# Kernel optimization log

Measured on AMD Instinct MI355X. Metric: run time of the kernel, lower is better.

## Reference

```python
import jax, jax.numpy as jnp
import numpy as np

NUM_WORDS = 256  # max word index + 1 (sentinel row NUM_WORDS used to drop non-first-occurrence scatters)


def setup_inputs() -> dict:
    key = jax.random.key(0)
    ks = jax.random.split(key, 8)
    B, S, H, R, D, C = 16, 512, 768, 8, 512, 27
    hidden_states = jax.random.normal(ks[0], (B, S, H), jnp.float32)
    word_ids = jnp.sort(jax.random.randint(ks[1], (B, S), 0, NUM_WORDS), axis=-1)
    relations_positions = jax.random.randint(ks[2], (B, R), 0, S)
    w_rel = jax.random.normal(ks[3], (H,), jnp.float32) / np.sqrt(H).astype(np.float32)
    b_rel = jnp.zeros((1,), jnp.float32)
    w1 = jax.random.normal(ks[4], (2 * H, D), jnp.float32) / np.sqrt(2 * H).astype(np.float32)
    b1 = jnp.zeros((D,), jnp.float32)
    w2 = jax.random.normal(ks[5], (D, C), jnp.float32) / np.sqrt(D).astype(np.float32)
    b2 = jnp.zeros((C,), jnp.float32)
    return dict(hidden_states=hidden_states, word_ids=word_ids,
                relations_positions=relations_positions,
                w_rel=w_rel, b_rel=b_rel, w1=w1, b1=b1, w2=w2, b2=b2)


def reference(hidden_states, word_ids, relations_positions, w_rel, b_rel, w1, b1, w2, b2):
    B, S, H = hidden_states.shape
    # relational logits: Linear(H, 1).squeeze(-1)  -> [B, S]
    rel_logits = jnp.einsum('bsh,h->bs', hidden_states, w_rel) + b_rel

    # first_hidden_states[i, w] = hidden_states[i, j] at the FIRST token j of word w
    # (torch loop keys on word_id != prev_word_id; word_ids are monotone per row)
    first_occ = jnp.concatenate(
        [jnp.ones((B, 1), bool), word_ids[:, 1:] != word_ids[:, :-1]], axis=1)
    tgt = jnp.where(first_occ, word_ids, NUM_WORDS)  # route non-first tokens to sentinel row
    batch_idx = jnp.arange(B)[:, None]
    first_hidden = (jnp.zeros((B, NUM_WORDS + 1, H), hidden_states.dtype)
                    .at[batch_idx, tgt].set(hidden_states))[:, :NUM_WORDS]  # [B, W, H]

    # gather relation token embeddings -> [B, R, H]
    rel_hidden = jnp.take_along_axis(
        hidden_states, relations_positions[:, :, None], axis=1)

    # concat([word_embed, rel_embed]) @ w1 == word_embed @ w1[:H] + rel_embed @ w1[H:]
    h_word = jnp.einsum('bwh,hd->bwd', first_hidden, w1[:H])   # [B, W, D]
    h_rel = jnp.einsum('brh,hd->brd', rel_hidden, w1[H:])      # [B, R, D]
    hmid = jax.nn.relu(h_word[:, None, :, :] + h_rel[:, :, None, :] + b1)  # [B, R, W, D]
    role_logits = jnp.einsum('brwd,dc->brwc', hmid, w2) + b2   # [B, R, W, C]

    return rel_logits, role_logits
```

## Files before the change

kernel.cpp:

```cpp
#include <hip/hip_runtime.h>
#include <hip/hip_bf16.h>

#define BB 16
#define SS 512
#define HH 768
#define RR 8
#define DD 512
#define CC 27
#define WW 256

typedef __attribute__((ext_vector_type(8))) short short8;
typedef __attribute__((ext_vector_type(4))) float f32x4;

union PKu { unsigned short us[8]; uint4 u4; short8 s8; };

__device__ __forceinline__ unsigned short f32_to_bf16_rne(float v) {
    unsigned int u = __float_as_uint(v);
    unsigned int r = u + 0x7fffu + ((u >> 16) & 1u);
    return (unsigned short)(r >> 16);
}
__device__ __forceinline__ float bf16_to_f32(unsigned short u) {
    return __uint_as_float(((unsigned int)u) << 16);
}

__device__ __forceinline__ void glds16(const void* g, void* l) {
    __builtin_amdgcn_global_load_lds(
        (const __attribute__((address_space(1))) unsigned int*)g,
        (__attribute__((address_space(3))) unsigned int*)l, 16, 0, 0);
}


__global__ __launch_bounds__(256) void k_front(
    const float* __restrict__ hidden, const int* __restrict__ word_ids,
    const int* __restrict__ relpos, const float4* __restrict__ wrel4,
    const float* __restrict__ b_rel, const float* __restrict__ w1,
    const float* __restrict__ w2, float* __restrict__ out0,
    unsigned short* __restrict__ first_hidden,
    unsigned short* __restrict__ rel_hidden,
    unsigned short* __restrict__ w1t, unsigned short* __restrict__ w2t) {
    int bid = blockIdx.x, t = threadIdx.x;
    if (bid < 2048) {
        int lane = t & 63;
        int row = bid * 4 + (t >> 6);
        const float4* hid4 = (const float4*)hidden + (size_t)row * (HH / 4);
        float4 v[3];
        float acc = 0.f;
#pragma unroll
        for (int j = 0; j < 3; ++j) {
            v[j] = hid4[j * 64 + lane];
            float4 w = wrel4[j * 64 + lane];
            acc += v[j].x * w.x + v[j].y * w.y + v[j].z * w.z + v[j].w * w.w;
        }
#pragma unroll
        for (int off = 32; off > 0; off >>= 1) acc += __shfl_xor(acc, off, 64);
        if (lane == 0) out0[row] = acc + b_rel[0];
        int wid = word_ids[row];
        int s = row & (SS - 1);
        int prev = (s == 0) ? -1 : word_ids[row - 1];
        if (wid != prev) {
            int b = row >> 9;
            unsigned short* dst = first_hidden + (size_t)(b * WW + wid) * HH;
#pragma unroll
            for (int j = 0; j < 3; ++j) {
                union { unsigned short us[4]; uint2 u2; } pk;
                pk.us[0] = f32_to_bf16_rne(v[j].x);
                pk.us[1] = f32_to_bf16_rne(v[j].y);
                pk.us[2] = f32_to_bf16_rne(v[j].z);
                pk.us[3] = f32_to_bf16_rne(v[j].w);
                *(uint2*)(dst + j * 256 + lane * 4) = pk.u2;
            }
        }
        return;
    }
    int x = bid - 2048;
    if (x < 192) {
        __shared__ unsigned short tile[64][72];
        int kt = x >> 3, nt = x & 7;
        int i = t >> 2, j4 = (t & 3) * 16;
        const float* src = w1 + (size_t)(kt * 64 + i) * DD + nt * 64 + j4;
#pragma unroll
        for (int v = 0; v < 4; ++v) {
            float4 f = *(const float4*)(src + v * 4);
            tile[i][j4 + v * 4 + 0] = f32_to_bf16_rne(f.x);
            tile[i][j4 + v * 4 + 1] = f32_to_bf16_rne(f.y);
            tile[i][j4 + v * 4 + 2] = f32_to_bf16_rne(f.z);
            tile[i][j4 + v * 4 + 3] = f32_to_bf16_rne(f.w);
        }
        __syncthreads();
        int jj = t >> 2, cb = (t & 3) * 16;
        union { unsigned short us[16]; uint4 u4[2]; } ov;
#pragma unroll
        for (int v = 0; v < 16; ++v) ov.us[v] = tile[cb + v][jj];
        unsigned short* dst = w1t + (size_t)(nt * 64 + jj) * (2 * HH) + kt * 64 + cb;
        *(uint4*)(dst) = ov.u4[0];
        *(uint4*)(dst + 8) = ov.u4[1];
    } else if (x == 192) {
        for (int idx = t; idx < 32 * DD; idx += 256) {
            int n = idx >> 9, k = idx & (DD - 1);
            float v = (n < CC) ? w2[(size_t)k * CC + n] : 0.f;
            w2t[n * DD + k] = f32_to_bf16_rne(v);
        }
    } else {
        __shared__ int pres[WW];
        int b = x - 193;
        pres[t] = 0;
        __syncthreads();
        for (int s = t; s < SS; s += 256) pres[word_ids[b * SS + s]] = 1;
        __syncthreads();
        if (!pres[t]) {
            uint4 z = {0u, 0u, 0u, 0u};
            unsigned short* dst = first_hidden + (size_t)(b * WW + t) * HH;
#pragma unroll 4
            for (int c = 0; c < 96; ++c) *(uint4*)(dst + c * 8) = z;
        }
        for (int idx = t; idx < 1024; idx += 256) {
            int rr = idx >> 7, c = idx & 127;
            if (c < 96) {
                int pos = relpos[b * RR + rr];
                const float* srow = hidden + (size_t)(b * SS + pos) * HH + c * 8;
                PKu pk;
#pragma unroll
                for (int e = 0; e < 8; ++e) pk.us[e] = f32_to_bf16_rne(srow[e]);
                *(uint4*)(rel_hidden + (size_t)(b * RR + rr) * HH + c * 8) = pk.u4;
            }
        }
    }
}

__global__ __launch_bounds__(256) void k_gemm(
    const unsigned short* __restrict__ first_hidden,
    const unsigned short* __restrict__ rel_hidden,
    const unsigned short* __restrict__ w1t, const float* __restrict__ b1,
    unsigned short* __restrict__ h_word, unsigned short* __restrict__ h_rel) {
    __shared__ __align__(16) unsigned char a_s[32768];
    __shared__ __align__(16) unsigned char b_s[16384];
    int bid = blockIdx.x;
    int nt, mt;
    if (bid < 256) {
        int xcd = bid & 7, k = bid >> 3;
        mt = xcd + 8 * (k & 3);
        nt = k >> 2;
    } else {
        mt = 32;
        nt = bid - 256;
    }
    bool isw = (mt < 32);
    const unsigned short* A = isw ? first_hidden : rel_hidden;
    unsigned short* C = isw ? h_word : h_rel;
    int kbase = isw ? 0 : HH;
    int m0 = isw ? mt * 128 : 0;
    int t = threadIdx.x;
    int wv = t >> 6, lane = t & 63;
    int wr = wv >> 1, wc = wv & 1;
    int q = lane >> 4, r = lane & 15;

    const unsigned char* aP[4];
    const unsigned char* bP[2];
    unsigned lofa[4], lofb[2];
#pragma unroll
    for (int j = 0; j < 4; ++j) {
        int ci = j * 256 + t;
        int row = ci >> 3, ch = ci & 7;
        int sc = ch ^ (row & 7);
        aP[j] = (const unsigned char*)A + (size_t)(m0 + row) * (HH * 2) + sc * 16;
        lofa[j] = ci * 16;
    }
#pragma unroll
    for (int j = 0; j < 2; ++j) {
        int ci = j * 256 + t;
        int row = ci >> 3, ch = ci & 7;
        int sc = ch ^ (row & 7);
        bP[j] = (const unsigned char*)w1t + (size_t)(nt * 64 + row) * (2 * HH * 2)
                + (size_t)kbase * 2 + sc * 16;
        lofb[j] = ci * 16;
    }
    int arow[4], brow[2];
#pragma unroll
    for (int mi = 0; mi < 4; ++mi) arow[mi] = wr * 64 + mi * 16 + r;
#pragma unroll
    for (int ni = 0; ni < 2; ++ni) brow[ni] = wc * 32 + ni * 16 + r;

    f32x4 acc[4][2];
#pragma unroll
    for (int mi = 0; mi < 4; ++mi)
#pragma unroll
        for (int ni = 0; ni < 2; ++ni) acc[mi][ni] = (f32x4){0.f, 0.f, 0.f, 0.f};

#pragma unroll
    for (int j = 0; j < 4; ++j) glds16(aP[j], a_s + lofa[j]);
#pragma unroll
    for (int j = 0; j < 2; ++j) glds16(bP[j], b_s + lofb[j]);
    __syncthreads();

    for (int kt = 0; kt < 12; ++kt) {
        if (kt < 11) {
            unsigned na = ((kt + 1) & 1) * 16384;
            unsigned nb = ((kt + 1) & 1) * 8192;
#pragma unroll
            for (int j = 0; j < 4; ++j) glds16(aP[j] + (kt + 1) * 128, a_s + na + lofa[j]);
#pragma unroll
            for (int j = 0; j < 2; ++j) glds16(bP[j] + (kt + 1) * 128, b_s + nb + lofb[j]);
        }
        unsigned ba = (kt & 1) * 16384;
        unsigned bb = (kt & 1) * 8192;
#pragma unroll
        for (int ks = 0; ks < 2; ++ks) {
            int c = ks * 4 + q;
            short8 bfr[2];
#pragma unroll
            for (int ni = 0; ni < 2; ++ni)
                bfr[ni] = *(const short8*)(b_s + bb + brow[ni] * 128 +
                            ((c ^ (brow[ni] & 7)) << 4));
#pragma unroll
            for (int mi = 0; mi < 4; ++mi) {
                short8 af = *(const short8*)(a_s + ba + arow[mi] * 128 +
                            ((c ^ (arow[mi] & 7)) << 4));
                acc[mi][0] = __builtin_amdgcn_mfma_f32_16x16x32_bf16(
                    af, bfr[0], acc[mi][0], 0, 0, 0);
                acc[mi][1] = __builtin_amdgcn_mfma_f32_16x16x32_bf16(
                    af, bfr[1], acc[mi][1], 0, 0, 0);
            }
        }
        __syncthreads();
    }
    float bias[2];
#pragma unroll
    for (int ni = 0; ni < 2; ++ni) {
        int n = nt * 64 + wc * 32 + ni * 16 + r;
        bias[ni] = isw ? b1[n] : 0.f;
    }
#pragma unroll
    for (int mi = 0; mi < 4; ++mi) {
        int m = m0 + wr * 64 + mi * 16 + q * 4;
#pragma unroll
        for (int ni = 0; ni < 2; ++ni) {
            int n = nt * 64 + wc * 32 + ni * 16 + r;
#pragma unroll
            for (int reg = 0; reg < 4; ++reg)
                C[(size_t)(m + reg) * DD + n] =
                    f32_to_bf16_rne(acc[mi][ni][reg] + bias[ni]);
        }
    }
}

__global__ __launch_bounds__(512) void k_role(
    const unsigned short* __restrict__ h_word, const unsigned short* __restrict__ h_rel,
    const unsigned short* __restrict__ w2t, const float* __restrict__ b2,
    float* __restrict__ out_role) {
    int wt = blockIdx.x;
    int b  = blockIdx.y;
    int t  = threadIdx.x;
    __shared__ __align__(16) unsigned char hw_s[16384];
    __shared__ float hr_s[RR][DD];
    __shared__ __align__(16) unsigned char w2_s[32768];
    int wv = t >> 6, lane = t & 63;
    {
#pragma unroll
        for (int i = 0; i < 2; ++i) {
            int row = wv * 2 + i;
            const unsigned short* src = h_word +
                (size_t)(b * WW + wt * 16 + row) * DD + ((lane ^ (row & 7)) * 8);
            glds16(src, hw_s + row * 1024 + lane * 16);
        }
    }
    {
#pragma unroll
        for (int i = 0; i < 4; ++i) {
            int row = wv * 4 + i;
            const unsigned short* src = w2t + row * DD + ((lane ^ (row & 7)) * 8);
            glds16(src, w2_s + row * 1024 + lane * 16);
        }
    }
    {
        int rr = t >> 6, c = t & 63;
        PKu hv;
        hv.u4 = *(const uint4*)(h_rel + (size_t)(b * RR + rr) * DD + c * 8);
        float4 o0, o1;
        o0.x = bf16_to_f32(hv.us[0]); o0.y = bf16_to_f32(hv.us[1]);
        o0.z = bf16_to_f32(hv.us[2]); o0.w = bf16_to_f32(hv.us[3]);
        o1.x = bf16_to_f32(hv.us[4]); o1.y = bf16_to_f32(hv.us[5]);
        o1.z = bf16_to_f32(hv.us[6]); o1.w = bf16_to_f32(hv.us[7]);
        *(float4*)&hr_s[rr][c * 8]     = o0;
        *(float4*)&hr_s[rr][c * 8 + 4] = o1;
    }
    __syncthreads();
    int q = lane >> 4, wl = lane & 15;
    int rr = wv;
    unsigned wlx = (wl & 7) << 4;
    f32x4 acc[2];
#pragma unroll
    for (int ni = 0; ni < 2; ++ni) acc[ni] = (f32x4){0.f, 0.f, 0.f, 0.f};

#pragma unroll 2
    for (int ks = 0; ks < DD / 32; ++ks) {
        int c = 4 * ks + q;
        short8 bfr[2];
#pragma unroll
        for (int ni = 0; ni < 2; ++ni) {
            int n = ni * 16 + wl;
            bfr[ni] = *(const short8*)(w2_s + n * 1024 + ((c ^ (n & 7)) << 4));
        }
        PKu hw;
        hw.u4 = *(const uint4*)(hw_s + wl * 1024 + ((unsigned)(c << 4) ^ wlx));
        const float* hrp = &hr_s[rr][ks * 32 + q * 8];
        float4 h0 = *(const float4*)(hrp);
        float4 h1 = *(const float4*)(hrp + 4);
        PKu pk;
        pk.us[0] = f32_to_bf16_rne(fmaxf(bf16_to_f32(hw.us[0]) + h0.x, 0.f));
        pk.us[1] = f32_to_bf16_rne(fmaxf(bf16_to_f32(hw.us[1]) + h0.y, 0.f));
        pk.us[2] = f32_to_bf16_rne(fmaxf(bf16_to_f32(hw.us[2]) + h0.z, 0.f));
        pk.us[3] = f32_to_bf16_rne(fmaxf(bf16_to_f32(hw.us[3]) + h0.w, 0.f));
        pk.us[4] = f32_to_bf16_rne(fmaxf(bf16_to_f32(hw.us[4]) + h1.x, 0.f));
        pk.us[5] = f32_to_bf16_rne(fmaxf(bf16_to_f32(hw.us[5]) + h1.y, 0.f));
        pk.us[6] = f32_to_bf16_rne(fmaxf(bf16_to_f32(hw.us[6]) + h1.z, 0.f));
        pk.us[7] = f32_to_bf16_rne(fmaxf(bf16_to_f32(hw.us[7]) + h1.w, 0.f));
#pragma unroll
        for (int ni = 0; ni < 2; ++ni)
            acc[ni] = __builtin_amdgcn_mfma_f32_16x16x32_bf16(
                pk.s8, bfr[ni], acc[ni], 0, 0, 0);
    }
#pragma unroll
    for (int ni = 0; ni < 2; ++ni) {
        int c = ni * 16 + wl;
        if (c < CC) {
#pragma unroll
            for (int reg = 0; reg < 4; ++reg) {
                int wg = wt * 16 + 4 * q + reg;
                out_role[(size_t)((b * RR + rr) * WW + wg) * CC + c] =
                    acc[ni][reg] + b2[c];
            }
        }
    }
}

extern "C" void kernel_launch(void* const* d_in, const int* in_sizes, int n_in,
                              void* d_out, int out_size, void* d_ws, size_t ws_size,
                              hipStream_t stream) {
    const float* hidden   = (const float*)d_in[0];
    const int*   word_ids = (const int*)d_in[1];
    const int*   relpos   = (const int*)d_in[2];
    const float* w_rel    = (const float*)d_in[3];
    const float* b_rel    = (const float*)d_in[4];
    const float* w1       = (const float*)d_in[5];
    const float* b1       = (const float*)d_in[6];
    const float* w2       = (const float*)d_in[7];
    const float* b2       = (const float*)d_in[8];

    float* out0 = (float*)d_out;
    float* out1 = out0 + BB * SS;

    unsigned short* first_hidden = (unsigned short*)d_ws;
    unsigned short* rel_hidden   = (unsigned short*)((char*)d_ws + 6291456);
    unsigned short* w1t          = (unsigned short*)((char*)d_ws + 6488064);
    unsigned short* w2t          = (unsigned short*)((char*)d_ws + 8060928);
    unsigned short* h_word       = (unsigned short*)((char*)d_ws + 8093696);
    unsigned short* h_rel        = (unsigned short*)((char*)d_ws + 12288000);

    k_front<<<2048 + 209, 256, 0, stream>>>(
        hidden, word_ids, relpos, (const float4*)w_rel, b_rel, w1, w2,
        out0, first_hidden, rel_hidden, w1t, w2t);
    k_gemm<<<264, 256, 0, stream>>>(
        first_hidden, rel_hidden, w1t, b1, h_word, h_rel);
    k_role<<<dim3(WW / 16, BB), 512, 0, stream>>>(h_word, h_rel, w2t, b2, out1);
}
```

Measured before the change: 41.63 us.

## Fuse first-token gather into word GEMM via index table, split prep kernel

Instead of scattering bf16 first-token rows into a materialized first_hidden buffer, a small prep kernel builds a per-batch first-occurrence index table. The word GEMM now reads fp32 hidden rows directly through that index, converts them to bf16 in registers and writes them into LDS, with zero rows for absent words. The rel-logit dot product moves into extra blocks of the GEMM launch. GEMM blocks grow to 512 threads with smaller per-wave tiles. This removes a 6 MB intermediate write and reread, but the GEMM A-operand path becomes a register-staged fp32 load instead of direct global-to-LDS loads.

```diff
diff --git a/kernel.cpp b/kernel.cpp
--- a/kernel.cpp
+++ b/kernel.cpp
@@ -22,57 +22,32 @@
 __device__ __forceinline__ float bf16_to_f32(unsigned short u) {
     return __uint_as_float(((unsigned int)u) << 16);
 }
-
 __device__ __forceinline__ void glds16(const void* g, void* l) {
     __builtin_amdgcn_global_load_lds(
         (const __attribute__((address_space(1))) unsigned int*)g,
         (__attribute__((address_space(3))) unsigned int*)l, 16, 0, 0);
 }
-
-
-__global__ __launch_bounds__(256) void k_front(
-    const float* __restrict__ hidden, const int* __restrict__ word_ids,
-    const int* __restrict__ relpos, const float4* __restrict__ wrel4,
-    const float* __restrict__ b_rel, const float* __restrict__ w1,
-    const float* __restrict__ w2, float* __restrict__ out0,
-    unsigned short* __restrict__ first_hidden,
+__device__ __forceinline__ uint4 pack8(float4 f0, float4 f1) {
+    PKu pk;
+    pk.us[0] = f32_to_bf16_rne(f0.x);
+    pk.us[1] = f32_to_bf16_rne(f0.y);
+    pk.us[2] = f32_to_bf16_rne(f0.z);
+    pk.us[3] = f32_to_bf16_rne(f0.w);
+    pk.us[4] = f32_to_bf16_rne(f1.x);
+    pk.us[5] = f32_to_bf16_rne(f1.y);
+    pk.us[6] = f32_to_bf16_rne(f1.z);
+    pk.us[7] = f32_to_bf16_rne(f1.w);
+    return pk.u4;
+}
+
+
+__global__ __launch_bounds__(256) void k_prep(
+    const float* __restrict__ w1, const float* __restrict__ w2,
+    const int* __restrict__ word_ids, const int* __restrict__ relpos,
+    const float* __restrict__ hidden, int* __restrict__ first_idx,
     unsigned short* __restrict__ rel_hidden,
     unsigned short* __restrict__ w1t, unsigned short* __restrict__ w2t) {
-    int bid = blockIdx.x, t = threadIdx.x;
-    if (bid < 2048) {
-        int lane = t & 63;
-        int row = bid * 4 + (t >> 6);
-        const float4* hid4 = (const float4*)hidden + (size_t)row * (HH / 4);
-        float4 v[3];
-        float acc = 0.f;
-#pragma unroll
-        for (int j = 0; j < 3; ++j) {
-            v[j] = hid4[j * 64 + lane];
-            float4 w = wrel4[j * 64 + lane];
-            acc += v[j].x * w.x + v[j].y * w.y + v[j].z * w.z + v[j].w * w.w;
-        }
-#pragma unroll
-        for (int off = 32; off > 0; off >>= 1) acc += __shfl_xor(acc, off, 64);
-        if (lane == 0) out0[row] = acc + b_rel[0];
-        int wid = word_ids[row];
-        int s = row & (SS - 1);
-        int prev = (s == 0) ? -1 : word_ids[row - 1];
-        if (wid != prev) {
-            int b = row >> 9;
-            unsigned short* dst = first_hidden + (size_t)(b * WW + wid) * HH;
-#pragma unroll
-            for (int j = 0; j < 3; ++j) {
-                union { unsigned short us[4]; uint2 u2; } pk;
-                pk.us[0] = f32_to_bf16_rne(v[j].x);
-                pk.us[1] = f32_to_bf16_rne(v[j].y);
-                pk.us[2] = f32_to_bf16_rne(v[j].z);
-                pk.us[3] = f32_to_bf16_rne(v[j].w);
-                *(uint2*)(dst + j * 256 + lane * 4) = pk.u2;
-            }
-        }
-        return;
-    }
-    int x = bid - 2048;
+    int x = blockIdx.x, t = threadIdx.x;
     if (x < 192) {
         __shared__ unsigned short tile[64][72];
         int kt = x >> 3, nt = x & 7;
@@ -101,128 +76,202 @@
             w2t[n * DD + k] = f32_to_bf16_rne(v);
         }
     } else {
-        __shared__ int pres[WW];
         int b = x - 193;
-        pres[t] = 0;
+        first_idx[b * WW + t] = -1;
         __syncthreads();
-        for (int s = t; s < SS; s += 256) pres[word_ids[b * SS + s]] = 1;
-        __syncthreads();
-        if (!pres[t]) {
-            uint4 z = {0u, 0u, 0u, 0u};
-            unsigned short* dst = first_hidden + (size_t)(b * WW + t) * HH;
-#pragma unroll 4
-            for (int c = 0; c < 96; ++c) *(uint4*)(dst + c * 8) = z;
-        }
-        for (int idx = t; idx < 1024; idx += 256) {
-            int rr = idx >> 7, c = idx & 127;
-            if (c < 96) {
-                int pos = relpos[b * RR + rr];
-                const float* srow = hidden + (size_t)(b * SS + pos) * HH + c * 8;
-                PKu pk;
-#pragma unroll
-                for (int e = 0; e < 8; ++e) pk.us[e] = f32_to_bf16_rne(srow[e]);
-                *(uint4*)(rel_hidden + (size_t)(b * RR + rr) * HH + c * 8) = pk.u4;
-            }
-        }
-    }
-}
-
-__global__ __launch_bounds__(256) void k_gemm(
-    const unsigned short* __restrict__ first_hidden,
+        for (int s = t; s < SS; s += 256) {
+            int wid = word_ids[b * SS + s];
+            int prev = (s == 0) ? -1 : word_ids[b * SS + s - 1];
+            if (wid != prev) first_idx[b * WW + wid] = s;
+        }
+        for (int idx = t; idx < RR * 96; idx += 256) {
+            int rr = idx / 96, c = idx % 96;
+            int pos = relpos[b * RR + rr];
+            const float* srow = hidden + (size_t)(b * SS + pos) * HH + c * 8;
+            float4 f0 = *(const float4*)(srow);
+            float4 f1 = *(const float4*)(srow + 4);
+            *(uint4*)(rel_hidden + (size_t)(b * RR + rr) * HH + c * 8) = pack8(f0, f1);
+        }
+    }
+}
+
+__global__ __launch_bounds__(512) void k_main(
+    const float* __restrict__ hidden, const float4* __restrict__ wrel4,
+    const float* __restrict__ b_rel, const int* __restrict__ first_idx,
     const unsigned short* __restrict__ rel_hidden,
     const unsigned short* __restrict__ w1t, const float* __restrict__ b1,
-    unsigned short* __restrict__ h_word, unsigned short* __restrict__ h_rel) {
+    float* __restrict__ out0, unsigned short* __restrict__ h_word,
+    unsigned short* __restrict__ h_rel) {
+    int bid = blockIdx.x, t = threadIdx.x;
+    int wv = t >> 6, lane = t & 63;
+    if (bid < 512) {
+#pragma unroll
+        for (int i = 0; i < 2; ++i) {
+            int row = bid * 16 + wv * 2 + i;
+            const float4* hid4 = (const float4*)hidden + (size_t)row * (HH / 4);
+            float acc = 0.f;
+#pragma unroll
+            for (int c = 0; c < 3; ++c) {
+                float4 v = hid4[c * 64 + lane];
+                float4 w = wrel4[c * 64 + lane];
+                acc += v.x * w.x + v.y * w.y + v.z * w.z + v.w * w.w;
+            }
+#pragma unroll
+            for (int off = 32; off > 0; off >>= 1) acc += __shfl_xor(acc, off, 64);
+            if (lane == 0) out0[row] = acc + b_rel[0];
+        }
+        return;
+    }
     __shared__ __align__(16) unsigned char a_s[32768];
     __shared__ __align__(16) unsigned char b_s[16384];
-    int bid = blockIdx.x;
+    int j = bid - 512;
     int nt, mt;
-    if (bid < 256) {
-        int xcd = bid & 7, k = bid >> 3;
+    if (j < 256) {
+        int xcd = j & 7, k = j >> 3;
         mt = xcd + 8 * (k & 3);
         nt = k >> 2;
-    } else {
-        mt = 32;
-        nt = bid - 256;
-    }
+    } else { mt = 32; nt = j - 256; }
     bool isw = (mt < 32);
-    const unsigned short* A = isw ? first_hidden : rel_hidden;
-    unsigned short* C = isw ? h_word : h_rel;
     int kbase = isw ? 0 : HH;
     int m0 = isw ? mt * 128 : 0;
-    int t = threadIdx.x;
-    int wv = t >> 6, lane = t & 63;
     int wr = wv >> 1, wc = wv & 1;
     int q = lane >> 4, r = lane & 15;
 
-    const unsigned char* aP[4];
-    const unsigned char* bP[2];
-    unsigned lofa[4], lofb[2];
-#pragma unroll
-    for (int j = 0; j < 4; ++j) {
-        int ci = j * 256 + t;
-        int row = ci >> 3, ch = ci & 7;
+    const unsigned char* bP;
+    unsigned lofb;
+    {
+        int row = t >> 3, ch = t & 7;
         int sc = ch ^ (row & 7);
-        aP[j] = (const unsigned char*)A + (size_t)(m0 + row) * (HH * 2) + sc * 16;
-        lofa[j] = ci * 16;
-    }
-#pragma unroll
-    for (int j = 0; j < 2; ++j) {
-        int ci = j * 256 + t;
-        int row = ci >> 3, ch = ci & 7;
-        int sc = ch ^ (row & 7);
-        bP[j] = (const unsigned char*)w1t + (size_t)(nt * 64 + row) * (2 * HH * 2)
-                + (size_t)kbase * 2 + sc * 16;
-        lofb[j] = ci * 16;
-    }
-    int arow[4], brow[2];
-#pragma unroll
-    for (int mi = 0; mi < 4; ++mi) arow[mi] = wr * 64 + mi * 16 + r;
+        bP = (const unsigned char*)w1t + (size_t)(nt * 64 + row) * (2 * HH * 2)
+             + (size_t)kbase * 2 + sc * 16;
+        lofb = t * 16;
+    }
+    int arow[2], brow[2];
+#pragma unroll
+    for (int mi = 0; mi < 2; ++mi) arow[mi] = wr * 32 + mi * 16 + r;
 #pragma unroll
     for (int ni = 0; ni < 2; ++ni) brow[ni] = wc * 32 + ni * 16 + r;
 
-    f32x4 acc[4][2];
-#pragma unroll
-    for (int mi = 0; mi < 4; ++mi)
+    f32x4 acc[2][2];
+#pragma unroll
+    for (int mi = 0; mi < 2; ++mi)
 #pragma unroll
         for (int ni = 0; ni < 2; ++ni) acc[mi][ni] = (f32x4){0.f, 0.f, 0.f, 0.f};
 
-#pragma unroll
-    for (int j = 0; j < 4; ++j) glds16(aP[j], a_s + lofa[j]);
-#pragma unroll
-    for (int j = 0; j < 2; ++j) glds16(bP[j], b_s + lofb[j]);
-    __syncthreads();
-
-    for (int kt = 0; kt < 12; ++kt) {
-        if (kt < 11) {
-            unsigned na = ((kt + 1) & 1) * 16384;
-            unsigned nb = ((kt + 1) & 1) * 8192;
-#pragma unroll
-            for (int j = 0; j < 4; ++j) glds16(aP[j] + (kt + 1) * 128, a_s + na + lofa[j]);
-#pragma unroll
-            for (int j = 0; j < 2; ++j) glds16(bP[j] + (kt + 1) * 128, b_s + nb + lofb[j]);
-        }
-        unsigned ba = (kt & 1) * 16384;
-        unsigned bb = (kt & 1) * 8192;
-#pragma unroll
-        for (int ks = 0; ks < 2; ++ks) {
-            int c = ks * 4 + q;
-            short8 bfr[2];
-#pragma unroll
-            for (int ni = 0; ni < 2; ++ni)
-                bfr[ni] = *(const short8*)(b_s + bb + brow[ni] * 128 +
-                            ((c ^ (brow[ni] & 7)) << 4));
-#pragma unroll
-            for (int mi = 0; mi < 4; ++mi) {
-                short8 af = *(const short8*)(a_s + ba + arow[mi] * 128 +
-                            ((c ^ (arow[mi] & 7)) << 4));
-                acc[mi][0] = __builtin_amdgcn_mfma_f32_16x16x32_bf16(
-                    af, bfr[0], acc[mi][0], 0, 0, 0);
-                acc[mi][1] = __builtin_amdgcn_mfma_f32_16x16x32_bf16(
-                    af, bfr[1], acc[mi][1], 0, 0, 0);
-            }
+    if (isw) {
+        const float* aSrc[2];
+        unsigned aw_off[2];
+        bool zro[2];
+#pragma unroll
+        for (int g = 0; g < 2; ++g) {
+            int ci = g * 512 + t;
+            int row = ci >> 3, ch = ci & 7;
+            int grow = m0 + row;
+            int src = first_idx[grow];
+            zro[g] = (src < 0);
+            aSrc[g] = hidden + (size_t)((grow >> 8) * SS + (src < 0 ? 0 : src)) * HH
+                      + ch * 8;
+            aw_off[g] = (unsigned)(row * 8 + (ch ^ (row & 7))) * 16;
+        }
+        uint4 zu4 = {0u, 0u, 0u, 0u};
+        glds16(bP, b_s + lofb);
+#pragma unroll
+        for (int g = 0; g < 2; ++g) {
+            uint4 av = zu4;
+            if (!zro[g])
+                av = pack8(*(const float4*)(aSrc[g]), *(const float4*)(aSrc[g] + 4));
+            *(uint4*)(a_s + aw_off[g]) = av;
         }
         __syncthreads();
-    }
+        for (int kt = 0; kt < 12; ++kt) {
+            float4 pf[2][2];
+            if (kt < 11) {
+#pragma unroll
+                for (int g = 0; g < 2; ++g)
+                    if (!zro[g]) {
+                        pf[g][0] = *(const float4*)(aSrc[g] + (kt + 1) * 64);
+                        pf[g][1] = *(const float4*)(aSrc[g] + (kt + 1) * 64 + 4);
+                    }
+                glds16(bP + (kt + 1) * 128, b_s + ((kt + 1) & 1) * 8192 + lofb);
+            }
+            unsigned ba = (kt & 1) * 16384;
+            unsigned bb = (kt & 1) * 8192;
+#pragma unroll
+            for (int ks = 0; ks < 2; ++ks) {
+                int c = ks * 4 + q;
+                short8 bfr[2];
+#pragma unroll
+                for (int ni = 0; ni < 2; ++ni)
+                    bfr[ni] = *(const short8*)(b_s + bb + brow[ni] * 128 +
+                                ((c ^ (brow[ni] & 7)) << 4));
+#pragma unroll
+                for (int mi = 0; mi < 2; ++mi) {
+                    short8 af = *(const short8*)(a_s + ba + arow[mi] * 128 +
+                                ((c ^ (arow[mi] & 7)) << 4));
+                    acc[mi][0] = __builtin_amdgcn_mfma_f32_16x16x32_bf16(
+                        af, bfr[0], acc[mi][0], 0, 0, 0);
+                    acc[mi][1] = __builtin_amdgcn_mfma_f32_16x16x32_bf16(
+                        af, bfr[1], acc[mi][1], 0, 0, 0);
+                }
+            }
+            if (kt < 11) {
+                unsigned na = ((kt + 1) & 1) * 16384;
+#pragma unroll
+                for (int g = 0; g < 2; ++g) {
+                    uint4 av = zro[g] ? zu4 : pack8(pf[g][0], pf[g][1]);
+                    *(uint4*)(a_s + na + aw_off[g]) = av;
+                }
+            }
+            __syncthreads();
+        }
+    } else {
+        const unsigned char* aP[2];
+        unsigned lofa[2];
+#pragma unroll
+        for (int g = 0; g < 2; ++g) {
+            int ci = g * 512 + t;
+            int row = ci >> 3, ch = ci & 7;
+            int sc = ch ^ (row & 7);
+            aP[g] = (const unsigned char*)rel_hidden + (size_t)row * (HH * 2) + sc * 16;
+            lofa[g] = ci * 16;
+        }
+#pragma unroll
+        for (int g = 0; g < 2; ++g) glds16(aP[g], a_s + lofa[g]);
+        glds16(bP, b_s + lofb);
+        __syncthreads();
+        for (int kt = 0; kt < 12; ++kt) {
+            if (kt < 11) {
+                unsigned na = ((kt + 1) & 1) * 16384;
+                unsigned nb = ((kt + 1) & 1) * 8192;
+#pragma unroll
+                for (int g = 0; g < 2; ++g)
+                    glds16(aP[g] + (kt + 1) * 128, a_s + na + lofa[g]);
+                glds16(bP + (kt + 1) * 128, b_s + nb + lofb);
+            }
+            unsigned ba = (kt & 1) * 16384;
+            unsigned bb = (kt & 1) * 8192;
+#pragma unroll
+            for (int ks = 0; ks < 2; ++ks) {
+                int c = ks * 4 + q;
+                short8 bfr[2];
+#pragma unroll
+                for (int ni = 0; ni < 2; ++ni)
+                    bfr[ni] = *(const short8*)(b_s + bb + brow[ni] * 128 +
+                                ((c ^ (brow[ni] & 7)) << 4));
+#pragma unroll
+                for (int mi = 0; mi < 2; ++mi) {
+                    short8 af = *(const short8*)(a_s + ba + arow[mi] * 128 +
+                                ((c ^ (arow[mi] & 7)) << 4));
+                    acc[mi][0] = __builtin_amdgcn_mfma_f32_16x16x32_bf16(
+                        af, bfr[0], acc[mi][0], 0, 0, 0);
+                    acc[mi][1] = __builtin_amdgcn_mfma_f32_16x16x32_bf16(
+                        af, bfr[1], acc[mi][1], 0, 0, 0);
+                }
+            }
+            __syncthreads();
+        }
+    }
+    unsigned short* C = isw ? h_word : h_rel;
     float bias[2];
 #pragma unroll
     for (int ni = 0; ni < 2; ++ni) {
@@ -230,8 +279,8 @@
         bias[ni] = isw ? b1[n] : 0.f;
     }
 #pragma unroll
-    for (int mi = 0; mi < 4; ++mi) {
-        int m = m0 + wr * 64 + mi * 16 + q * 4;
+    for (int mi = 0; mi < 2; ++mi) {
+        int m = m0 + wr * 32 + mi * 16 + q * 4;
 #pragma unroll
         for (int ni = 0; ni < 2; ++ni) {
             int n = nt * 64 + wc * 32 + ni * 16 + r;
@@ -254,25 +303,21 @@
     __shared__ float hr_s[RR][DD];
     __shared__ __align__(16) unsigned char w2_s[32768];
     int wv = t >> 6, lane = t & 63;
+#pragma unroll
+    for (int i = 0; i < 2; ++i) {
+        int row = wv * 2 + i;
+        const unsigned short* src = h_word +
+            (size_t)(b * WW + wt * 16 + row) * DD + ((lane ^ (row & 7)) * 8);
+        glds16(src, hw_s + row * 1024 + lane * 16);
+    }
+#pragma unroll
+    for (int i = 0; i < 4; ++i) {
+        int row = wv * 4 + i;
+        const unsigned short* src = w2t + row * DD + ((lane ^ (row & 7)) * 8);
+        glds16(src, w2_s + row * 1024 + lane * 16);
+    }
     {
-#pragma unroll
-        for (int i = 0; i < 2; ++i) {
-            int row = wv * 2 + i;
-            const unsigned short* src = h_word +
-                (size_t)(b * WW + wt * 16 + row) * DD + ((lane ^ (row & 7)) * 8);
-            glds16(src, hw_s + row * 1024 + lane * 16);
-        }
-    }
-    {
-#pragma unroll
-        for (int i = 0; i < 4; ++i) {
-            int row = wv * 4 + i;
-            const unsigned short* src = w2t + row * DD + ((lane ^ (row & 7)) * 8);
-            glds16(src, w2_s + row * 1024 + lane * 16);
-        }
-    }
-    {
-        int rr = t >> 6, c = t & 63;
+        int rr = wv, c = lane;
         PKu hv;
         hv.u4 = *(const uint4*)(h_rel + (size_t)(b * RR + rr) * DD + c * 8);
         float4 o0, o1;
@@ -349,17 +394,17 @@
     float* out0 = (float*)d_out;
     float* out1 = out0 + BB * SS;
 
-    unsigned short* first_hidden = (unsigned short*)d_ws;
-    unsigned short* rel_hidden   = (unsigned short*)((char*)d_ws + 6291456);
-    unsigned short* w1t          = (unsigned short*)((char*)d_ws + 6488064);
-    unsigned short* w2t          = (unsigned short*)((char*)d_ws + 8060928);
-    unsigned short* h_word       = (unsigned short*)((char*)d_ws + 8093696);
-    unsigned short* h_rel        = (unsigned short*)((char*)d_ws + 12288000);
-
-    k_front<<<2048 + 209, 256, 0, stream>>>(
-        hidden, word_ids, relpos, (const float4*)w_rel, b_rel, w1, w2,
-        out0, first_hidden, rel_hidden, w1t, w2t);
-    k_gemm<<<264, 256, 0, stream>>>(
-        first_hidden, rel_hidden, w1t, b1, h_word, h_rel);
+    int*            first_idx  = (int*)d_ws;
+    unsigned short* rel_hidden = (unsigned short*)((char*)d_ws + 16384);
+    unsigned short* w1t        = (unsigned short*)((char*)d_ws + 212992);
+    unsigned short* w2t        = (unsigned short*)((char*)d_ws + 1785856);
+    unsigned short* h_word     = (unsigned short*)((char*)d_ws + 1818624);
+    unsigned short* h_rel      = (unsigned short*)((char*)d_ws + 6012928);
+
+    k_prep<<<209, 256, 0, stream>>>(w1, w2, word_ids, relpos, hidden,
+                                    first_idx, rel_hidden, w1t, w2t);
+    k_main<<<776, 512, 0, stream>>>(hidden, (const float4*)w_rel, b_rel,
+                                    first_idx, rel_hidden, w1t, b1,
+                                    out0, h_word, h_rel);
     k_role<<<dim3(WW / 16, BB), 512, 0, stream>>>(h_word, h_rel, w2t, b2, out1);
 }
```

After: 45.60 us. +9.5%, slower.
